# Performance work log

Measured on AMD Instinct MI355X. Metric: run time of the kernel, lower is better.

## Reference

```python
import jax, jax.numpy as jnp
import numpy as np

B = 4096
E = 1024   # input_size (embedding)
H = 1024   # hidden_size
C = 1024   # context_vector_size
D = E + H + C  # combined_vector_size


def setup_inputs() -> dict:
    key = jax.random.key(0)
    ks = jax.random.split(key, 20)
    s_gate = 1.0 / np.sqrt(D)
    s_c = 1.0 / np.sqrt(C)
    s_h = 1.0 / np.sqrt(H)
    s_e = 1.0 / np.sqrt(E)
    return {
        "previous_embedded_caption": jax.random.normal(ks[0], (B, E), jnp.float32),
        "previous_hidden_state": jax.random.normal(ks[1], (B, H), jnp.float32),
        "previous_cell_state": jax.random.normal(ks[2], (B, H), jnp.float32),
        "current_context_vector": jax.random.normal(ks[3], (B, C), jnp.float32),
        "Wi": jax.random.uniform(ks[4], (H, D), jnp.float32, -s_gate, s_gate),
        "bi": jax.random.uniform(ks[5], (H,), jnp.float32, -s_gate, s_gate),
        "Wf": jax.random.uniform(ks[6], (H, D), jnp.float32, -s_gate, s_gate),
        "bf": jax.random.uniform(ks[7], (H,), jnp.float32, -s_gate, s_gate),
        "Wo": jax.random.uniform(ks[8], (H, D), jnp.float32, -s_gate, s_gate),
        "bo": jax.random.uniform(ks[9], (H,), jnp.float32, -s_gate, s_gate),
        "Wg": jax.random.uniform(ks[10], (H, D), jnp.float32, -s_gate, s_gate),
        "bg": jax.random.uniform(ks[11], (H,), jnp.float32, -s_gate, s_gate),
        "Wc": jax.random.uniform(ks[12], (E, C), jnp.float32, -s_c, s_c),
        "bc": jax.random.uniform(ks[13], (E,), jnp.float32, -s_c, s_c),
        "Wh": jax.random.uniform(ks[14], (E, H), jnp.float32, -s_h, s_h),
        "bh": jax.random.uniform(ks[15], (E,), jnp.float32, -s_h, s_h),
        "Wp": jax.random.uniform(ks[16], (E, E), jnp.float32, -s_e, s_e),
        "bp": jax.random.uniform(ks[17], (E,), jnp.float32, -s_e, s_e),
    }


def reference(previous_embedded_caption, previous_hidden_state, previous_cell_state,
              current_context_vector, Wi, bi, Wf, bf, Wo, bo, Wg, bg,
              Wc, bc, Wh, bh, Wp, bp):
    # combined vector [B, D]
    combined = jnp.concatenate(
        [previous_embedded_caption, previous_hidden_state, current_context_vector], axis=1)
    i = jax.nn.sigmoid(combined @ Wi.T + bi)
    f = jax.nn.sigmoid(combined @ Wf.T + bf)
    o = jax.nn.sigmoid(combined @ Wo.T + bo)
    g = jnp.tanh(combined @ Wg.T + bg)
    cell = f * previous_cell_state + i * g           # [B, H]
    hidden = o * jnp.tanh(cell)                      # [B, H]
    resid = previous_embedded_caption + (hidden @ Wh.T + bh) + (current_context_vector @ Wc.T + bc)
    prediction = resid @ Wp.T + bp                   # [B, E]
    return (prediction, hidden, cell)
```

## Files before the change

kernel.cpp:

```cpp
#include <hip/hip_runtime.h>
#include <stdint.h>

#define BATCH 4096
#define EHC   1024
#define DCOMB 3072
#define NTOT  ((size_t)BATCH * EHC)
#define WGATE ((size_t)EHC * DCOMB)
#define WSML  ((size_t)EHC * EHC)

#define BK 64

typedef __bf16 bf16x8 __attribute__((ext_vector_type(8)));
typedef float  f32x4  __attribute__((ext_vector_type(4)));

__device__ inline unsigned short f2b(float f) {
    unsigned int x = __float_as_uint(f);
    unsigned int r = (x + 0x7fffu + ((x >> 16) & 1u)) >> 16;
    return (unsigned short)r;
}
__device__ inline float sigmoid_f(float x) { return 1.0f / (1.0f + __expf(-x)); }
__device__ inline float tanh_f(float x) {
    float xa = fminf(fmaxf(x, -15.0f), 15.0f);
    float e = __expf(2.0f * xa);
    return (e - 1.0f) / (e + 1.0f);
}

__device__ inline void load16(const void* g, void* l) {
    __builtin_amdgcn_global_load_lds(
        (const __attribute__((address_space(1))) void*)g,
        (__attribute__((address_space(3))) void*)l, 16, 0, 0);
}

__global__ __launch_bounds__(256)
void cvt_all(const float* __restrict__ s0, const float* __restrict__ s1,
             const float* __restrict__ s2, const float* __restrict__ s3,
             const float* __restrict__ s4, const float* __restrict__ s5,
             const float* __restrict__ s6, const float* __restrict__ s7,
             const float* __restrict__ s8, const float* __restrict__ s9,
             short* __restrict__ dst)
{
    const unsigned b = blockIdx.x;
    const float* src = s0; unsigned st = 0;
    if (b >= 2048)  { src = s1; st = 2048;  }
    if (b >= 4096)  { src = s2; st = 4096;  }
    if (b >= 6144)  { src = s3; st = 6144;  }
    if (b >= 7680)  { src = s4; st = 7680;  }
    if (b >= 9216)  { src = s5; st = 9216;  }
    if (b >= 10752) { src = s6; st = 10752; }
    if (b >= 12288) { src = s7; st = 12288; }
    if (b >= 12800) { src = s8; st = 12800; }
    if (b >= 13312) { src = s9; st = 13312; }
    size_t soff = ((size_t)(b - st) * 2048) + (size_t)threadIdx.x * 8;
    size_t doff = ((size_t)b * 2048) + (size_t)threadIdx.x * 8;
    float4 a = *(const float4*)(src + soff);
    float4 c = *(const float4*)(src + soff + 4);
    uint4 v;
    v.x = (unsigned)f2b(a.x) | ((unsigned)f2b(a.y) << 16);
    v.y = (unsigned)f2b(a.z) | ((unsigned)f2b(a.w) << 16);
    v.z = (unsigned)f2b(c.x) | ((unsigned)f2b(c.y) << 16);
    v.w = (unsigned)f2b(c.z) | ((unsigned)f2b(c.w) << 16);
    *(uint4*)(dst + doff) = v;
}

__global__ __launch_bounds__(512, 2)
void gemm_gates8(const short* __restrict__ A0, const short* __restrict__ A1,
                 const short* __restrict__ A2, const short* __restrict__ W,
                 const float* __restrict__ b0, const float* __restrict__ b1,
                 const float* __restrict__ b2, const float* __restrict__ b3,
                 const float* __restrict__ pcell,
                 float* __restrict__ cell_o, float* __restrict__ hid_o,
                 short* __restrict__ hid_b)
{
    const int nblk = blockIdx.x;
    const int mblk = blockIdx.y;
    const int tid  = threadIdx.x;
    const int lane = tid & 63;
    const int wave = tid >> 6;
    const int wm   = wave >> 1;
    const int wn   = wave & 1;
    const int l15  = lane & 15;
    const int l4   = lane >> 4;

    __shared__ short lds[65536];

    int aoff[2][2], adst[2][2];
#pragma unroll
    for (int u = 0; u < 2; u++)
#pragma unroll
        for (int j = 0; j < 2; j++) {
            int ca = u * 1024 + j * 512 + tid;
            int r  = ca >> 3, q = ca & 7;
            int qg = q ^ (r & 7);
            aoff[u][j] = (mblk * 256 + r) * 1024 + qg * 8;
            adst[u][j] = ca * 8;
        }
    int boff[2][2], bdst[2][2];
#pragma unroll
    for (int u = 0; u < 2; u++)
#pragma unroll
        for (int j = 0; j < 2; j++) {
            int c2 = j * 512 + tid;
            int g  = u * 2 + (c2 >> 9);
            int rb = (c2 >> 3) & 63;
            int q  = c2 & 7;
            int qg = q ^ (rb & 7);
            boff[u][j] = g * (int)WGATE + (nblk * 64 + rb) * 3072 + qg * 8;
            bdst[u][j] = 16384 + (u * 1024 + c2) * 8;
        }

    int a_ld[2][4], b_ld[2][2];
#pragma unroll
    for (int s = 0; s < 2; s++) {
        int qf = s * 4 + l4;
#pragma unroll
        for (int mi = 0; mi < 4; mi++) {
            int rowA = wm * 64 + mi * 16 + l15;
            a_ld[s][mi] = (rowA * 8 + (qf ^ (rowA & 7))) * 8;
        }
#pragma unroll
        for (int ni = 0; ni < 2; ni++) {
            int rowB = wn * 32 + ni * 16 + l15;
            b_ld[s][ni] = 16384 + (rowB * 8 + (qf ^ (rowB & 7))) * 8;
        }
    }

    f32x4 acc[4][4][2];
#pragma unroll
    for (int g = 0; g < 4; g++)
#pragma unroll
        for (int mi = 0; mi < 4; mi++)
#pragma unroll
            for (int ni = 0; ni < 2; ni++) acc[g][mi][ni] = (f32x4){0.f, 0.f, 0.f, 0.f};

#pragma unroll
    for (int u = 0; u < 2; u++)
#pragma unroll
        for (int j = 0; j < 2; j++)
            load16(A0 + aoff[u][j], lds + adst[u][j]);
#pragma unroll
    for (int u = 0; u < 2; u++)
#pragma unroll
        for (int j = 0; j < 2; j++)
            load16(W + boff[u][j], lds + bdst[u][j]);
    asm volatile("s_waitcnt vmcnt(2)" ::: "memory");
    __builtin_amdgcn_s_barrier();

    const int KT = DCOMB / BK;
#pragma unroll 1
    for (int t = 0; t < KT; ++t) {
        const int  P   = (t & 1) * 32768;
        const bool pf  = (t + 1 < KT);
        const int  k1  = (t + 1) * 64;
        const int  Pn  = ((t + 1) & 1) * 32768;
        const int  ac1 = k1 & 1023;
        const int  sn  = k1 >> 10;
        const short* An = (sn == 0) ? A0 : (sn == 1) ? A1 : A2;

        bf16x8 af[2][4];
#pragma unroll
        for (int g = 0; g < 4; g++) {
            if (g == 0) {
#pragma unroll
                for (int s = 0; s < 2; s++)
#pragma unroll
                    for (int mi = 0; mi < 4; mi++)
                        af[s][mi] = *(const bf16x8*)(lds + P + a_ld[s][mi]);
            }
            bf16x8 bv[2][2];
#pragma unroll
            for (int s = 0; s < 2; s++)
#pragma unroll
                for (int ni = 0; ni < 2; ni++)
                    bv[s][ni] = *(const bf16x8*)(lds + P + b_ld[s][ni] + g * 4096);

            if (pf) {
                if (g < 2) {
#pragma unroll
                    for (int j = 0; j < 2; j++)
                        load16(An + aoff[g][j] + ac1, lds + Pn + adst[g][j]);
                } else {
#pragma unroll
                    for (int j = 0; j < 2; j++)
                        load16(W + boff[g - 2][j] + k1, lds + Pn + bdst[g - 2][j]);
                }
            }

            if (g == 1) asm volatile("s_waitcnt vmcnt(4)" ::: "memory");
            if (g == 3) asm volatile("s_waitcnt vmcnt(2)" ::: "memory");

            __builtin_amdgcn_s_barrier();
            asm volatile("s_waitcnt lgkmcnt(0)" ::: "memory");
            __builtin_amdgcn_s_setprio(1);
#pragma unroll
            for (int s = 0; s < 2; s++)
#pragma unroll
                for (int mi = 0; mi < 4; mi++)
#pragma unroll
                    for (int ni = 0; ni < 2; ni++)
                        acc[g][mi][ni] = __builtin_amdgcn_mfma_f32_16x16x32_bf16(
                            af[s][mi], bv[s][ni], acc[g][mi][ni], 0, 0, 0);
            __builtin_amdgcn_s_setprio(0);
            __builtin_amdgcn_s_barrier();
        }
    }

#pragma unroll
    for (int ni = 0; ni < 2; ni++) {
        const int col = nblk * 64 + wn * 32 + ni * 16 + l15;
        const float bi_ = b0[col], bf_ = b1[col], bo_ = b2[col], bg_ = b3[col];
#pragma unroll
        for (int mi = 0; mi < 4; mi++) {
#pragma unroll
            for (int r = 0; r < 4; r++) {
                const size_t row = (size_t)(mblk * 256 + wm * 64 + mi * 16 + l4 * 4 + r);
                const size_t idx = row * 1024 + col;
                float ai  = fminf(fmaxf(acc[0][mi][ni][r] + bi_, -30.f), 30.f);
                float af_ = fminf(fmaxf(acc[1][mi][ni][r] + bf_, -30.f), 30.f);
                float ao  = fminf(fmaxf(acc[2][mi][ni][r] + bo_, -30.f), 30.f);
                float ag  = fminf(fmaxf(acc[3][mi][ni][r] + bg_, -30.f), 30.f);
                float ig = sigmoid_f(ai), fg = sigmoid_f(af_);
                float og = sigmoid_f(ao), gg = tanh_f(ag);
                float c = fg * pcell[idx] + ig * gg;
                float h = og * tanh_f(c);
                cell_o[idx] = c;
                hid_o[idx]  = h;
                hid_b[idx]  = (short)f2b(h);
            }
        }
    }
}

template <int MODE>
__global__ __launch_bounds__(256, 2)
void gemm_fused(const short* __restrict__ A0, const short* __restrict__ A1,
                const short* __restrict__ A2,
                const short* __restrict__ W0, const short* __restrict__ W1,
                const short* __restrict__ W2, const short* __restrict__ W3,
                const float* __restrict__ b0, const float* __restrict__ b1,
                const float* __restrict__ b2, const float* __restrict__ b3,
                const float* __restrict__ extra,
                void* __restrict__ outv, float* __restrict__ out2,
                short* __restrict__ out3)
{
    constexpr int NG  = (MODE == 1) ? 4 : 1;
    constexpr int BMT = (MODE == 1) ? 128 : 64;
    constexpr int BNT = 64;
    constexpr int MI  = BMT / 32;
    constexpr int NI  = BNT / 32;
    constexpr int AI  = BMT / 32;
    constexpr int BI  = BNT / 32;
    constexpr int WMH = BMT / 2;
    constexpr int BSZ = BNT * BK;

    const int nblk = blockIdx.x;
    const int mblk = blockIdx.y;
    const int tid  = threadIdx.x;
    const int lane = tid & 63;
    const int wave = tid >> 6;
    const int wm = wave >> 1;
    const int wn = wave & 1;
    const int l15 = lane & 15;
    const int l4  = lane >> 4;

    __shared__ short As[BMT * BK];
    __shared__ short Bs[NG * BSZ];

    const int K = (MODE == 1) ? DCOMB : (MODE == 2 ? 2048 : 1024);
    const int wstride = (MODE == 1) ? DCOMB : 1024;
    const int wrowbase = nblk * BNT;

    int aoff[AI], woff[BI];
#pragma unroll
    for (int j = 0; j < AI; j++) {
        int c  = j * 256 + tid;
        int r  = c >> 3;
        int qg = (c & 7) ^ (r & 7);
        aoff[j] = (mblk * BMT + r) * 1024 + qg * 8;
    }
#pragma unroll
    for (int j = 0; j < BI; j++) {
        int c  = j * 256 + tid;
        int r  = c >> 3;
        int qg = (c & 7) ^ (r & 7);
        woff[j] = (wrowbase + r) * wstride + qg * 8;
    }

    int a_ld[2][MI], b_ld[2][NI];
#pragma unroll
    for (int s = 0; s < 2; s++) {
        int q = s * 4 + l4;
#pragma unroll
        for (int i = 0; i < MI; i++) {
            int rowA = wm * WMH + i * 16 + l15;
            a_ld[s][i] = (rowA * 8 + (q ^ (rowA & 7))) * 8;
        }
#pragma unroll
        for (int i = 0; i < NI; i++) {
            int rowB = wn * 32 + i * 16 + l15;
            b_ld[s][i] = (rowB * 8 + (q ^ (rowB & 7))) * 8;
        }
    }

    f32x4 acc[NG][MI][NI];
#pragma unroll
    for (int g = 0; g < NG; g++)
#pragma unroll
        for (int i = 0; i < MI; i++)
#pragma unroll
            for (int j = 0; j < NI; j++) acc[g][i][j] = (f32x4){0.f, 0.f, 0.f, 0.f};

    const int KT = K / BK;
    for (int kt = 0; kt < KT; ++kt) {
        const int k0   = kt * BK;
        const int seg  = (MODE == 3) ? 0 : (k0 >> 10);
        const int acol = k0 & 1023;
        const short* Aseg = (seg == 0) ? A0 : (seg == 1) ? A1 : A2;

        __syncthreads();
#pragma unroll
        for (int j = 0; j < AI; j++)
            load16(Aseg + aoff[j] + acol, &As[(j * 256 + tid) * 8]);
        if (MODE == 1) {
            const short* Wg4[4] = {W0, W1, W2, W3};
#pragma unroll
            for (int g = 0; g < 4; g++)
#pragma unroll
                for (int j = 0; j < BI; j++)
                    load16(Wg4[g] + woff[j] + k0, &Bs[g * BSZ + (j * 256 + tid) * 8]);
        } else {
            const short* Wt = (seg == 0) ? W0 : W1;
#pragma unroll
            for (int j = 0; j < BI; j++)
                load16(Wt + woff[j] + acol, &Bs[(j * 256 + tid) * 8]);
        }
        __syncthreads();

#pragma unroll
        for (int s = 0; s < 2; s++) {
            bf16x8 af[MI];
#pragma unroll
            for (int i = 0; i < MI; i++) af[i] = *(const bf16x8*)(As + a_ld[s][i]);
#pragma unroll
            for (int g = 0; g < NG; g++) {
                bf16x8 bv[NI];
#pragma unroll
                for (int i = 0; i < NI; i++)
                    bv[i] = *(const bf16x8*)(Bs + g * BSZ + b_ld[s][i]);
#pragma unroll
                for (int mi = 0; mi < MI; mi++)
#pragma unroll
                    for (int ni = 0; ni < NI; ni++)
                        acc[g][mi][ni] = __builtin_amdgcn_mfma_f32_16x16x32_bf16(
                            af[mi], bv[ni], acc[g][mi][ni], 0, 0, 0);
            }
        }
    }

#pragma unroll
    for (int ni = 0; ni < NI; ni++) {
        const int col = nblk * BNT + wn * 32 + ni * 16 + l15;
        if (MODE == 1) {
            const float bi_ = b0[col], bf_ = b1[col], bo_ = b2[col], bg_ = b3[col];
#pragma unroll
            for (int mi = 0; mi < MI; mi++) {
#pragma unroll
                for (int r = 0; r < 4; r++) {
                    const size_t row = (size_t)(mblk * BMT + wm * WMH + mi * 16 + l4 * 4 + r);
                    const size_t idx = row * 1024 + col;
                    float ai = fminf(fmaxf(acc[0][mi][ni][r] + bi_, -30.f), 30.f);
                    float af_ = fminf(fmaxf(acc[1][mi][ni][r] + bf_, -30.f), 30.f);
                    float ao = fminf(fmaxf(acc[2][mi][ni][r] + bo_, -30.f), 30.f);
                    float ag = fminf(fmaxf(acc[3][mi][ni][r] + bg_, -30.f), 30.f);
                    float ig = sigmoid_f(ai), fg = sigmoid_f(af_);
                    float og = sigmoid_f(ao), gg = tanh_f(ag);
                    float c = fg * extra[idx] + ig * gg;
                    float h = og * tanh_f(c);
                    ((float*)outv)[idx] = c;
                    out2[idx] = h;
                    out3[idx] = (short)f2b(h);
                }
            }
        } else {
            float bias_v = (MODE == 2) ? (b0[col] + b1[col]) : b0[col];
#pragma unroll
            for (int mi = 0; mi < MI; mi++) {
#pragma unroll
                for (int r = 0; r < 4; r++) {
                    const size_t row = (size_t)(mblk * BMT + wm * WMH + mi * 16 + l4 * 4 + r);
                    const size_t idx = row * 1024 + col;
                    float v = acc[0][mi][ni][r] + bias_v;
                    if (MODE == 2) {
                        v += extra[idx];
                        ((short*)outv)[idx] = (short)f2b(v);
                    } else {
                        ((float*)outv)[idx] = v;
                    }
                }
            }
        }
    }
}

extern "C" void kernel_launch(void* const* d_in, const int* in_sizes, int n_in,
                              void* d_out, int out_size, void* d_ws, size_t ws_size,
                              hipStream_t stream)
{
    const float* emb  = (const float*)d_in[0];
    const float* hid  = (const float*)d_in[1];
    const float* pcel = (const float*)d_in[2];
    const float* ctx  = (const float*)d_in[3];
    const float* Wi = (const float*)d_in[4];   const float* bi = (const float*)d_in[5];
    const float* Wf = (const float*)d_in[6];   const float* bf_ = (const float*)d_in[7];
    const float* Wo = (const float*)d_in[8];   const float* bo = (const float*)d_in[9];
    const float* Wg = (const float*)d_in[10];  const float* bg = (const float*)d_in[11];
    const float* Wc = (const float*)d_in[12];  const float* bc = (const float*)d_in[13];
    const float* Wh = (const float*)d_in[14];  const float* bh = (const float*)d_in[15];
    const float* Wp = (const float*)d_in[16];  const float* bp = (const float*)d_in[17];

    float* out      = (float*)d_out;
    float* pred     = out;
    float* hidden_o = out + NTOT;
    float* cell_o   = out + 2 * NTOT;

    short* ws = (short*)d_ws;
    short* w_emb  = ws;
    short* w_hid  = ws + NTOT;
    short* w_ctx  = ws + 2 * NTOT;
    short* w_Wg4  = ws + 3 * NTOT;
    short* w_Wh   = w_Wg4 + 4 * WGATE;
    short* w_Wc   = w_Wh + WSML;
    short* w_Wp   = w_Wc + WSML;
    short* w_hidb = w_Wp + WSML;
    short* w_res  = w_hidb + NTOT;

    dim3 blk(256, 1, 1);
    const short* np16 = nullptr;
    const float* npf  = nullptr;

    hipLaunchKernelGGL(cvt_all, dim3(13824), blk, 0, stream,
                       emb, hid, ctx, Wi, Wf, Wo, Wg, Wh, Wc, Wp, ws);

    hipLaunchKernelGGL(gemm_gates8, dim3(16, 16), dim3(512, 1, 1), 0, stream,
                       w_emb, w_hid, w_ctx, w_Wg4,
                       bi, bf_, bo, bg, pcel,
                       cell_o, hidden_o, w_hidb);
    hipLaunchKernelGGL((gemm_fused<2>), dim3(16, 64), blk, 0, stream,
                       w_hidb, w_ctx, np16, w_Wh, w_Wc, np16, np16,
                       bh, bc, npf, npf, emb, (void*)w_res, (float*)nullptr, (short*)nullptr);
    hipLaunchKernelGGL((gemm_fused<3>), dim3(16, 64), blk, 0, stream,
                       w_res, np16, np16, w_Wp, np16, np16, np16,
                       bp, npf, npf, npf, npf, (void*)pred, (float*)nullptr, (short*)nullptr);
}
```

Before: 336.8 us.

## Software-pipeline LDS fragment loads in gates GEMM and retile smaller GEMMs

The gates GEMM inner loop is restructured so each gate phase prefetches the next phase's B fragments, and at the last phase the next tile's A and B fragments, from LDS into double-buffered registers. This overlaps LDS reads with MFMA work and drops the per-phase lgkmcnt(0) wait. Separately, the two smaller GEMMs switch to 128-row tiles with a remapped block order meant to improve L2 reuse, and the unused MODE 1 code is removed. The extra register fragments raise register pressure, and the larger tiles halve the grid.

```diff
diff --git a/kernel.cpp b/kernel.cpp
--- a/kernel.cpp
+++ b/kernel.cpp
@@ -62,6 +62,65 @@
     *(uint4*)(dst + doff) = v;
 }
 
+template <int G>
+__device__ __forceinline__ void gates_phase(
+    bool pf, const short* __restrict__ An, const short* __restrict__ W,
+    const int (&aoff)[2][2], const int (&adst)[2][2],
+    const int (&boff)[2][2], const int (&bdst)[2][2],
+    int k1, int ac1, short* lds, int P, int Pn,
+    const int (&a_ld)[2][4], const int (&b_ld)[2][2],
+    bf16x8 (&af)[2][4], bf16x8 (&cur)[2][2], bf16x8 (&nxt)[2][2],
+    f32x4 (&accg)[4][2])
+{
+    if (pf) {
+        if (G < 2) {
+#pragma unroll
+            for (int j = 0; j < 2; j++)
+                load16(An + aoff[G][j] + ac1, lds + Pn + adst[G][j]);
+        } else {
+#pragma unroll
+            for (int j = 0; j < 2; j++)
+                load16(W + boff[G - 2][j] + k1, lds + Pn + bdst[G - 2][j]);
+        }
+    }
+    if (G == 1) {
+        if (pf) asm volatile("s_waitcnt vmcnt(4)" ::: "memory");
+        else    asm volatile("s_waitcnt vmcnt(0)" ::: "memory");
+    }
+    if (G == 3 && pf) asm volatile("s_waitcnt vmcnt(2)" ::: "memory");
+    asm volatile("s_barrier" ::: "memory");
+    if (G < 3) {
+#pragma unroll
+        for (int s = 0; s < 2; s++)
+#pragma unroll
+            for (int ni = 0; ni < 2; ni++)
+                nxt[s][ni] = *(const bf16x8*)(lds + P + b_ld[s][ni] + (G + 1) * 4096);
+    }
+    __builtin_amdgcn_s_setprio(1);
+#pragma unroll
+    for (int s = 0; s < 2; s++)
+#pragma unroll
+        for (int mi = 0; mi < 4; mi++)
+#pragma unroll
+            for (int ni = 0; ni < 2; ni++)
+                accg[mi][ni] = __builtin_amdgcn_mfma_f32_16x16x32_bf16(
+                    af[s][mi], cur[s][ni], accg[mi][ni], 0, 0, 0);
+    __builtin_amdgcn_s_setprio(0);
+    if (G == 3 && pf) {
+#pragma unroll
+        for (int s = 0; s < 2; s++)
+#pragma unroll
+            for (int mi = 0; mi < 4; mi++)
+                af[s][mi] = *(const bf16x8*)(lds + Pn + a_ld[s][mi]);
+#pragma unroll
+        for (int s = 0; s < 2; s++)
+#pragma unroll
+            for (int ni = 0; ni < 2; ni++)
+                nxt[s][ni] = *(const bf16x8*)(lds + Pn + b_ld[s][ni]);
+    }
+    __builtin_amdgcn_s_barrier();
+}
+
 __global__ __launch_bounds__(512, 2)
 void gemm_gates8(const short* __restrict__ A0, const short* __restrict__ A1,
                  const short* __restrict__ A2, const short* __restrict__ W,
@@ -143,65 +202,39 @@
         for (int j = 0; j < 2; j++)
             load16(W + boff[u][j], lds + bdst[u][j]);
     asm volatile("s_waitcnt vmcnt(2)" ::: "memory");
-    __builtin_amdgcn_s_barrier();
+    asm volatile("s_barrier" ::: "memory");
+
+    bf16x8 af[2][4], bvA[2][2], bvB[2][2];
+#pragma unroll
+    for (int s = 0; s < 2; s++)
+#pragma unroll
+        for (int mi = 0; mi < 4; mi++)
+            af[s][mi] = *(const bf16x8*)(lds + a_ld[s][mi]);
+#pragma unroll
+    for (int s = 0; s < 2; s++)
+#pragma unroll
+        for (int ni = 0; ni < 2; ni++)
+            bvA[s][ni] = *(const bf16x8*)(lds + b_ld[s][ni]);
 
     const int KT = DCOMB / BK;
 #pragma unroll 1
     for (int t = 0; t < KT; ++t) {
         const int  P   = (t & 1) * 32768;
+        const int  Pn  = P ^ 32768;
         const bool pf  = (t + 1 < KT);
         const int  k1  = (t + 1) * 64;
-        const int  Pn  = ((t + 1) & 1) * 32768;
         const int  ac1 = k1 & 1023;
         const int  sn  = k1 >> 10;
         const short* An = (sn == 0) ? A0 : (sn == 1) ? A1 : A2;
 
-        bf16x8 af[2][4];
-#pragma unroll
-        for (int g = 0; g < 4; g++) {
-            if (g == 0) {
-#pragma unroll
-                for (int s = 0; s < 2; s++)
-#pragma unroll
-                    for (int mi = 0; mi < 4; mi++)
-                        af[s][mi] = *(const bf16x8*)(lds + P + a_ld[s][mi]);
-            }
-            bf16x8 bv[2][2];
-#pragma unroll
-            for (int s = 0; s < 2; s++)
-#pragma unroll
-                for (int ni = 0; ni < 2; ni++)
-                    bv[s][ni] = *(const bf16x8*)(lds + P + b_ld[s][ni] + g * 4096);
-
-            if (pf) {
-                if (g < 2) {
-#pragma unroll
-                    for (int j = 0; j < 2; j++)
-                        load16(An + aoff[g][j] + ac1, lds + Pn + adst[g][j]);
-                } else {
-#pragma unroll
-                    for (int j = 0; j < 2; j++)
-                        load16(W + boff[g - 2][j] + k1, lds + Pn + bdst[g - 2][j]);
-                }
-            }
-
-            if (g == 1) asm volatile("s_waitcnt vmcnt(4)" ::: "memory");
-            if (g == 3) asm volatile("s_waitcnt vmcnt(2)" ::: "memory");
-
-            __builtin_amdgcn_s_barrier();
-            asm volatile("s_waitcnt lgkmcnt(0)" ::: "memory");
-            __builtin_amdgcn_s_setprio(1);
-#pragma unroll
-            for (int s = 0; s < 2; s++)
-#pragma unroll
-                for (int mi = 0; mi < 4; mi++)
-#pragma unroll
-                    for (int ni = 0; ni < 2; ni++)
-                        acc[g][mi][ni] = __builtin_amdgcn_mfma_f32_16x16x32_bf16(
-                            af[s][mi], bv[s][ni], acc[g][mi][ni], 0, 0, 0);
-            __builtin_amdgcn_s_setprio(0);
-            __builtin_amdgcn_s_barrier();
-        }
+        gates_phase<0>(pf, An, W, aoff, adst, boff, bdst, k1, ac1, lds, P, Pn,
+                       a_ld, b_ld, af, bvA, bvB, acc[0]);
+        gates_phase<1>(pf, An, W, aoff, adst, boff, bdst, k1, ac1, lds, P, Pn,
+                       a_ld, b_ld, af, bvB, bvA, acc[1]);
+        gates_phase<2>(pf, An, W, aoff, adst, boff, bdst, k1, ac1, lds, P, Pn,
+                       a_ld, b_ld, af, bvA, bvB, acc[2]);
+        gates_phase<3>(pf, An, W, aoff, adst, boff, bdst, k1, ac1, lds, P, Pn,
+                       a_ld, b_ld, af, bvB, bvA, acc[3]);
     }
 
 #pragma unroll
@@ -242,8 +275,8 @@
                 void* __restrict__ outv, float* __restrict__ out2,
                 short* __restrict__ out3)
 {
-    constexpr int NG  = (MODE == 1) ? 4 : 1;
-    constexpr int BMT = (MODE == 1) ? 128 : 64;
+    constexpr int NG  = 1;
+    constexpr int BMT = 128;
     constexpr int BNT = 64;
     constexpr int MI  = BMT / 32;
     constexpr int NI  = BNT / 32;
@@ -252,8 +285,11 @@
     constexpr int WMH = BMT / 2;
     constexpr int BSZ = BNT * BK;
 
-    const int nblk = blockIdx.x;
-    const int mblk = blockIdx.y;
+    int flat = blockIdx.y * 16 + blockIdx.x;
+    flat = (flat & 7) * 64 + (flat >> 3);
+    const int nblk = flat & 15;
+    const int mblk = flat >> 4;
+
     const int tid  = threadIdx.x;
     const int lane = tid & 63;
     const int wave = tid >> 6;
@@ -265,8 +301,8 @@
     __shared__ short As[BMT * BK];
     __shared__ short Bs[NG * BSZ];
 
-    const int K = (MODE == 1) ? DCOMB : (MODE == 2 ? 2048 : 1024);
-    const int wstride = (MODE == 1) ? DCOMB : 1024;
+    const int K = (MODE == 2) ? 2048 : 1024;
+    const int wstride = 1024;
     const int wrowbase = nblk * BNT;
 
     int aoff[AI], woff[BI];
@@ -314,20 +350,13 @@
         const int k0   = kt * BK;
         const int seg  = (MODE == 3) ? 0 : (k0 >> 10);
         const int acol = k0 & 1023;
-        const short* Aseg = (seg == 0) ? A0 : (seg == 1) ? A1 : A2;
+        const short* Aseg = (seg == 0) ? A0 : A1;
 
         __syncthreads();
 #pragma unroll
         for (int j = 0; j < AI; j++)
             load16(Aseg + aoff[j] + acol, &As[(j * 256 + tid) * 8]);
-        if (MODE == 1) {
-            const short* Wg4[4] = {W0, W1, W2, W3};
-#pragma unroll
-            for (int g = 0; g < 4; g++)
-#pragma unroll
-                for (int j = 0; j < BI; j++)
-                    load16(Wg4[g] + woff[j] + k0, &Bs[g * BSZ + (j * 256 + tid) * 8]);
-        } else {
+        {
             const short* Wt = (seg == 0) ? W0 : W1;
 #pragma unroll
             for (int j = 0; j < BI; j++)
@@ -340,61 +369,35 @@
             bf16x8 af[MI];
 #pragma unroll
             for (int i = 0; i < MI; i++) af[i] = *(const bf16x8*)(As + a_ld[s][i]);
-#pragma unroll
-            for (int g = 0; g < NG; g++) {
-                bf16x8 bv[NI];
-#pragma unroll
-                for (int i = 0; i < NI; i++)
-                    bv[i] = *(const bf16x8*)(Bs + g * BSZ + b_ld[s][i]);
-#pragma unroll
-                for (int mi = 0; mi < MI; mi++)
-#pragma unroll
-                    for (int ni = 0; ni < NI; ni++)
-                        acc[g][mi][ni] = __builtin_amdgcn_mfma_f32_16x16x32_bf16(
-                            af[mi], bv[ni], acc[g][mi][ni], 0, 0, 0);
-            }
+            bf16x8 bv[NI];
+#pragma unroll
+            for (int i = 0; i < NI; i++)
+                bv[i] = *(const bf16x8*)(Bs + b_ld[s][i]);
+#pragma unroll
+            for (int mi = 0; mi < MI; mi++)
+#pragma unroll
+                for (int ni = 0; ni < NI; ni++)
+                    acc[0][mi][ni] = __builtin_amdgcn_mfma_f32_16x16x32_bf16(
+                        af[mi], bv[ni], acc[0][mi][ni], 0, 0, 0);
         }
     }
 
 #pragma unroll
     for (int ni = 0; ni < NI; ni++) {
         const int col = nblk * BNT + wn * 32 + ni * 16 + l15;
-        if (MODE == 1) {
-            const float bi_ = b0[col], bf_ = b1[col], bo_ = b2[col], bg_ = b3[col];
-#pragma unroll
-            for (int mi = 0; mi < MI; mi++) {
-#pragma unroll
-                for (int r = 0; r < 4; r++) {
-                    const size_t row = (size_t)(mblk * BMT + wm * WMH + mi * 16 + l4 * 4 + r);
-                    const size_t idx = row * 1024 + col;
-                    float ai = fminf(fmaxf(acc[0][mi][ni][r] + bi_, -30.f), 30.f);
-                    float af_ = fminf(fmaxf(acc[1][mi][ni][r] + bf_, -30.f), 30.f);
-                    float ao = fminf(fmaxf(acc[2][mi][ni][r] + bo_, -30.f), 30.f);
-                    float ag = fminf(fmaxf(acc[3][mi][ni][r] + bg_, -30.f), 30.f);
-                    float ig = sigmoid_f(ai), fg = sigmoid_f(af_);
-                    float og = sigmoid_f(ao), gg = tanh_f(ag);
-                    float c = fg * extra[idx] + ig * gg;
-                    float h = og * tanh_f(c);
-                    ((float*)outv)[idx] = c;
-                    out2[idx] = h;
-                    out3[idx] = (short)f2b(h);
-                }
-            }
-        } else {
-            float bias_v = (MODE == 2) ? (b0[col] + b1[col]) : b0[col];
-#pragma unroll
-            for (int mi = 0; mi < MI; mi++) {
-#pragma unroll
-                for (int r = 0; r < 4; r++) {
-                    const size_t row = (size_t)(mblk * BMT + wm * WMH + mi * 16 + l4 * 4 + r);
-                    const size_t idx = row * 1024 + col;
-                    float v = acc[0][mi][ni][r] + bias_v;
-                    if (MODE == 2) {
-                        v += extra[idx];
-                        ((short*)outv)[idx] = (short)f2b(v);
-                    } else {
-                        ((float*)outv)[idx] = v;
-                    }
+        float bias_v = (MODE == 2) ? (b0[col] + b1[col]) : b0[col];
+#pragma unroll
+        for (int mi = 0; mi < MI; mi++) {
+#pragma unroll
+            for (int r = 0; r < 4; r++) {
+                const size_t row = (size_t)(mblk * BMT + wm * WMH + mi * 16 + l4 * 4 + r);
+                const size_t idx = row * 1024 + col;
+                float v = acc[0][mi][ni][r] + bias_v;
+                if (MODE == 2) {
+                    v += extra[idx];
+                    ((short*)outv)[idx] = (short)f2b(v);
+                } else {
+                    ((float*)outv)[idx] = v;
                 }
             }
         }
@@ -444,10 +447,10 @@
                        w_emb, w_hid, w_ctx, w_Wg4,
                        bi, bf_, bo, bg, pcel,
                        cell_o, hidden_o, w_hidb);
-    hipLaunchKernelGGL((gemm_fused<2>), dim3(16, 64), blk, 0, stream,
+    hipLaunchKernelGGL((gemm_fused<2>), dim3(16, 32), blk, 0, stream,
                        w_hidb, w_ctx, np16, w_Wh, w_Wc, np16, np16,
                        bh, bc, npf, npf, emb, (void*)w_res, (float*)nullptr, (short*)nullptr);
-    hipLaunchKernelGGL((gemm_fused<3>), dim3(16, 64), blk, 0, stream,
+    hipLaunchKernelGGL((gemm_fused<3>), dim3(16, 32), blk, 0, stream,
                        w_res, np16, np16, w_Wp, np16, np16, np16,
                        bp, npf, npf, npf, npf, (void*)pred, (float*)nullptr, (short*)nullptr);
 }
```

Measured after the change: 335.6 us. No clear change (-0.3%).
